# Optimization experiments

Hardware: AMD Instinct MI355X
Metric: run time of the kernel (lower is better)

The kernel has to match this reference:

```python
import jax, jax.numpy as jnp
import numpy as np

B, T, C = 2, 2048, 1024
H, D = 16, 64


def setup_inputs() -> dict:
    key = jax.random.key(0)
    k1, k2, k3 = jax.random.split(key, 3)
    x = jax.random.normal(k1, (B, T, C), dtype=jnp.float32)
    w_qkv = jax.random.normal(k2, (C, 3 * H * D), dtype=jnp.float32) * (C ** -0.5)
    w_proj = jax.random.normal(k3, (H * D, C), dtype=jnp.float32) * ((H * D) ** -0.5)
    sink_logit = jnp.zeros((H,), dtype=jnp.float32)
    return {"x": x, "w_qkv": w_qkv, "w_proj": w_proj, "sink_logit": sink_logit}


def reference(x, w_qkv, w_proj, sink_logit):
    b, t, c = x.shape
    qkv = x @ w_qkv                                  # [B,T,3HD]
    q, k, v = jnp.split(qkv, 3, axis=-1)
    # [B,H,T,D]
    q = q.reshape(b, t, H, D).transpose(0, 2, 1, 3)
    k = k.reshape(b, t, H, D).transpose(0, 2, 1, 3)
    v = v.reshape(b, t, H, D).transpose(0, 2, 1, 3)

    scale = 1.0 / jnp.sqrt(jnp.asarray(D, dtype=x.dtype))
    scores = jnp.einsum('bhqd,bhkd->bhqk', q, k) * scale   # [B,H,T,T]
    neg_inf = jnp.finfo(x.dtype).min
    causal = jnp.tril(jnp.ones((t, t), dtype=bool))
    scores = jnp.where(causal[None, None], scores, neg_inf)

    # sink column: per-head learnable logit b (added post-scale, V is zero)
    sink = jnp.broadcast_to(sink_logit.reshape(1, H, 1, 1), (b, H, t, 1)).astype(x.dtype)
    aug = jnp.concatenate([sink, scores], axis=-1)          # [B,H,T,T+1]
    attn = jax.nn.softmax(aug, axis=-1)
    # sink V is zero, so drop the sink column for the value contraction
    y = jnp.einsum('bhqk,bhkd->bhqd', attn[..., 1:], v)     # [B,H,T,D]
    y = y.transpose(0, 2, 1, 3).reshape(b, t, H * D)
    return y @ w_proj
```

## Files before the change

### kernel.cpp

```cpp
#include <hip/hip_runtime.h>
#include <hip/hip_bf16.h>
#include <stdint.h>

#define B_ 2
#define T_ 2048
#define C_ 1024
#define H_ 16
#define D_ 64

typedef __attribute__((ext_vector_type(8))) short short8;
typedef __attribute__((ext_vector_type(4))) float floatx4;

__device__ __forceinline__ float bf2f(uint16_t b) {
    return __uint_as_float(((uint32_t)b) << 16);
}
__device__ __forceinline__ uint16_t f2b(float f) {
    __hip_bfloat16 h = __float2bfloat16(f);
    return *(uint16_t*)&h;
}
__device__ __forceinline__ float exp2v(float x) {
    float r;
    asm("v_exp_f32 %0, %1" : "=v"(r) : "v"(x));
    return r;
}
__device__ __forceinline__ uint32_t cvtpk(float lo, float hi) {
    uint32_t r;
    asm("v_cvt_pk_bf16_f32 %0, %1, %2" : "=v"(r) : "v"(lo), "v"(hi));
    return r;
}
__device__ __forceinline__ void glds16(const uint16_t* g, uint16_t* l) {
    __builtin_amdgcn_global_load_lds(
        (const __attribute__((address_space(1))) uint32_t*)g,
        (__attribute__((address_space(3))) uint32_t*)l, 16, 0, 0);
}

__global__ void prep(const float* __restrict__ x, uint16_t* __restrict__ x_c,
                     const float* __restrict__ w_qkv, uint16_t* __restrict__ wt_qkv,
                     const float* __restrict__ w_proj, uint16_t* __restrict__ wt_proj) {
    __shared__ uint16_t tile[32][33];
    int id = blockIdx.x;
    int tid = threadIdx.x;
    if (id < 4096) {
        int i = (id * 256 + tid) * 4;
        float4 v = *(const float4*)(x + i);
        x_c[i + 0] = f2b(v.x);
        x_c[i + 1] = f2b(v.y);
        x_c[i + 2] = f2b(v.z);
        x_c[i + 3] = f2b(v.w);
        return;
    }
    const float* in;
    uint16_t* out;
    int R, W, bx, by;
    if (id < 7168) {
        int tb = id - 4096;
        in = w_qkv; out = wt_qkv; R = 1024; W = 3072;
        bx = tb % 96; by = tb / 96;
    } else {
        int tb = id - 7168;
        in = w_proj; out = wt_proj; R = 1024; W = 1024;
        bx = tb & 31; by = tb >> 5;
    }
    int tx = tid & 31, ty = tid >> 5;
    int c0 = bx * 32, r0 = by * 32;
    #pragma unroll
    for (int i = 0; i < 32; i += 8)
        tile[ty + i][tx] = f2b(in[(size_t)(r0 + ty + i) * W + (c0 + tx)]);
    __syncthreads();
    #pragma unroll
    for (int i = 0; i < 32; i += 8)
        out[(size_t)(c0 + ty + i) * R + (r0 + tx)] = tile[tx][ty + i];
}

template <bool OUT_F32>
__global__ __launch_bounds__(256, 3)
void gemm_bt(const uint16_t* __restrict__ A, const uint16_t* __restrict__ Bt,
             void* __restrict__ Cv, int M, int N, int K) {
    __shared__ uint16_t As[3][128][32];
    __shared__ uint16_t Bs[3][128][32];
    int tid = threadIdx.x;
    int w = tid >> 6, lane = tid & 63;
    int quad = lane >> 4, l16 = lane & 15;
    int wr = (w >> 1) * 64, wc = (w & 1) * 64;

    int nwg = gridDim.x;
    int wg = (blockIdx.x & 7) * (nwg >> 3) + (blockIdx.x >> 3);
    int nby = N >> 7;
    int row0 = (wg / nby) * 128;
    int col0 = (wg % nby) * 128;

    int sr = w * 32 + (lane >> 2);
    int gsc = ((lane & 3) ^ ((lane >> 2) & 3)) * 8;
    uint16_t* lA0 = &As[0][sr][(lane & 3) * 8];
    uint16_t* lB0 = &Bs[0][sr][(lane & 3) * 8];
    const uint16_t* gA = A + (size_t)(row0 + sr) * K + gsc;
    const uint16_t* gB = Bt + (size_t)(col0 + sr) * K + gsc;

    floatx4 acc[4][4];
    #pragma unroll
    for (int i = 0; i < 4; i++)
        #pragma unroll
        for (int j = 0; j < 4; j++)
            acc[i][j] = (floatx4){0.f, 0.f, 0.f, 0.f};

#define STAGE3_(bs_, t_)                                                    \
    {                                                                       \
        const uint16_t* ga_ = gA + (size_t)(t_) * 32;                       \
        const uint16_t* gb_ = gB + (size_t)(t_) * 32;                       \
        uint16_t* la_ = lA0 + (bs_) * 4096;                                 \
        uint16_t* lb_ = lB0 + (bs_) * 4096;                                 \
        glds16(ga_, la_);                                                   \
        glds16(ga_ + 16 * K, la_ + 512);                                    \
        glds16(gb_, lb_);                                                   \
        glds16(gb_ + 16 * K, lb_ + 512);                                    \
    }

    int NT = K >> 5;
    STAGE3_(0, 0);
    STAGE3_(1, 1);
    asm volatile("s_waitcnt vmcnt(4)" ::: "memory");
    __builtin_amdgcn_s_barrier();

    const uint16_t* Ab = &As[0][0][0];
    const uint16_t* Bb = &Bs[0][0][0];
    int s = (quad ^ (l16 & 3)) * 8;
    int bc = 0, bs = 2;
    for (int t = 0; t < NT; ++t) {
        if (t + 2 < NT) STAGE3_(bs, t + 2);
        __builtin_amdgcn_sched_barrier(0);
        const uint16_t* Ac = Ab + bc * 4096;
        const uint16_t* Bc = Bb + bc * 4096;
        short8 af[4], bfr[4];
        #pragma unroll
        for (int i = 0; i < 4; i++)
            af[i] = *(const short8*)&Ac[(wr + i * 16 + l16) * 32 + s];
        #pragma unroll
        for (int j = 0; j < 4; j++)
            bfr[j] = *(const short8*)&Bc[(wc + j * 16 + l16) * 32 + s];
        #pragma unroll
        for (int i = 0; i < 4; i++)
            #pragma unroll
            for (int j = 0; j < 4; j++)
                acc[i][j] = __builtin_amdgcn_mfma_f32_16x16x32_bf16(
                    af[i], bfr[j], acc[i][j], 0, 0, 0);
        if (t + 2 < NT) {
            asm volatile("s_waitcnt vmcnt(4)" ::: "memory");
        } else {
            asm volatile("s_waitcnt vmcnt(0)" ::: "memory");
        }
        __builtin_amdgcn_s_barrier();
        bc = (bc == 2) ? 0 : bc + 1;
        bs = (bs == 2) ? 0 : bs + 1;
    }
#undef STAGE3_

    #pragma unroll
    for (int i = 0; i < 4; i++) {
        #pragma unroll
        for (int j = 0; j < 4; j++) {
            int rbase = row0 + wr + i * 16 + quad * 4;
            int cg = col0 + wc + j * 16 + l16;
            #pragma unroll
            for (int r = 0; r < 4; r++) {
                if (OUT_F32)
                    ((float*)Cv)[(size_t)(rbase + r) * N + cg] = acc[i][j][r];
                else
                    ((uint16_t*)Cv)[(size_t)(rbase + r) * N + cg] = f2b(acc[i][j][r]);
            }
        }
    }
}

__global__ __launch_bounds__(256, 2)
void attn_mfma(const uint16_t* __restrict__ qkv,
               const float* __restrict__ sink,
               uint16_t* __restrict__ y) {
    __shared__ uint16_t Ks[2][64][72];
    __shared__ uint16_t Vt[2][64][72];
    __shared__ uint16_t Pl[4][32][72];

    int tid = threadIdx.x;
    int w = tid >> 6, lane = tid & 63;
    int quad = lane >> 4, l16 = lane & 15;

    int id = blockIdx.x;
    int pair = id >> 5, bh = id & 31;
    int b = bh >> 4, h = bh & 15;
    int hi = 31 - pair, lo = pair;
    int q0s[2];
    q0s[0] = hi * 64 + w * 16;
    q0s[1] = lo * 64 + w * 16;
    int ktiles = hi + 1;
    int myk1 = lo + 1;

    const uint16_t* qkv_b = qkv + (size_t)b * T_ * 3072;

    const float QSC = 0.125f * 1.44269504f;
    short8 qf[2][2];
    #pragma unroll
    for (int qt = 0; qt < 2; qt++) {
        int qrow = q0s[qt] + l16;
        #pragma unroll
        for (int kd = 0; kd < 2; kd++) {
            uint4 raw = *(const uint4*)(qkv_b + (size_t)qrow * 3072 + h * 64 +
                                        kd * 32 + quad * 8);
            const uint16_t* rp = (const uint16_t*)&raw;
            short8 f;
            #pragma unroll
            for (int j = 0; j < 8; j++)
                f[j] = (short)f2b(bf2f(rp[j]) * QSC);
            qf[qt][kd] = f;
        }
    }

    float m_s[2], l_s[2];
    m_s[0] = m_s[1] = sink[h] * 1.44269504f;
    l_s[0] = l_s[1] = 1.0f;
    floatx4 acc_o[2][4];
    #pragma unroll
    for (int qt = 0; qt < 2; qt++)
        #pragma unroll
        for (int dt = 0; dt < 4; dt++)
            acc_o[qt][dt] = (floatx4){0.f, 0.f, 0.f, 0.f};

    int t2 = tid >> 3;
    int dg = tid & 7;
    const uint16_t* kgp = qkv_b + 1024 + h * 64 + (size_t)(2 * t2) * 3072 + dg * 8;
    const uint16_t* vgp = kgp + 1024;
    int vcw = 2 * (t2 ^ (4 * dg));

    uint4 kr0 = *(const uint4*)(kgp);
    uint4 kr1 = *(const uint4*)(kgp + 3072);
    uint4 vr0 = *(const uint4*)(vgp);
    uint4 vr1 = *(const uint4*)(vgp + 3072);
    {
        *(uint4*)&Ks[0][2 * t2][dg * 8] = kr0;
        *(uint4*)&Ks[0][2 * t2 + 1][dg * 8] = kr1;
        const uint16_t* a0 = (const uint16_t*)&vr0;
        const uint16_t* a1 = (const uint16_t*)&vr1;
        #pragma unroll
        for (int j = 0; j < 8; j++)
            *(uint32_t*)&Vt[0][dg * 8 + j][vcw] =
                (uint32_t)a0[j] | ((uint32_t)a1[j] << 16);
    }
    if (ktiles > 1) {
        kr0 = *(const uint4*)(kgp + 64 * 3072);
        kr1 = *(const uint4*)(kgp + 64 * 3072 + 3072);
        vr0 = *(const uint4*)(vgp + 64 * 3072);
        vr1 = *(const uint4*)(vgp + 64 * 3072 + 3072);
    }
    __syncthreads();

    for (int kt = 0; kt < ktiles; kt++) {
        int cur = kt & 1;
        if (kt + 1 < ktiles) {
            *(uint4*)&Ks[cur ^ 1][2 * t2][dg * 8] = kr0;
            *(uint4*)&Ks[cur ^ 1][2 * t2 + 1][dg * 8] = kr1;
            const uint16_t* a0 = (const uint16_t*)&vr0;
            const uint16_t* a1 = (const uint16_t*)&vr1;
            #pragma unroll
            for (int j = 0; j < 8; j++)
                *(uint32_t*)&Vt[cur ^ 1][dg * 8 + j][vcw] =
                    (uint32_t)a0[j] | ((uint32_t)a1[j] << 16);
        }
        if (kt + 2 < ktiles) {
            size_t off = (size_t)(kt + 2) * 64 * 3072;
            kr0 = *(const uint4*)(kgp + off);
            kr1 = *(const uint4*)(kgp + off + 3072);
            vr0 = *(const uint4*)(vgp + off);
            vr1 = *(const uint4*)(vgp + off + 3072);
        }
        short8 kf[4][2];
        #pragma unroll
        for (int rt = 0; rt < 4; rt++) {
            kf[rt][0] = *(const short8*)&Ks[cur][rt * 16 + l16][quad * 8];
            kf[rt][1] = *(const short8*)&Ks[cur][rt * 16 + l16][32 + quad * 8];
        }
        short8 vf[2][4];
        #pragma unroll
        for (int kb = 0; kb < 2; kb++)
            #pragma unroll
            for (int dt = 0; dt < 4; dt++) {
                int d = dt * 16 + l16;
                int col = 2 * (((kb * 16) + quad * 4) ^ (4 * (d >> 3)));
                vf[kb][dt] = *(const short8*)&Vt[cur][d][col];
            }
        #pragma unroll
        for (int qt = 0; qt < 2; qt++) {
            if (qt == 1 && kt >= myk1) continue;
            floatx4 acc_s[4];
            #pragma unroll
            for (int rt = 0; rt < 4; rt++)
                acc_s[rt] = (floatx4){0.f, 0.f, 0.f, 0.f};
            #pragma unroll
            for (int rt = 0; rt < 4; rt++) {
                acc_s[rt] = __builtin_amdgcn_mfma_f32_16x16x32_bf16(
                    kf[rt][0], qf[qt][0], acc_s[rt], 0, 0, 0);
                acc_s[rt] = __builtin_amdgcn_mfma_f32_16x16x32_bf16(
                    kf[rt][1], qf[qt][1], acc_s[rt], 0, 0, 0);
            }
            int dqt = (qt == 0) ? hi : lo;
            if (kt == dqt) {
                int qg = q0s[qt] + l16;
                #pragma unroll
                for (int rt = 0; rt < 4; rt++) {
                    int kg = kt * 64 + rt * 16 + quad * 4;
                    #pragma unroll
                    for (int r = 0; r < 4; r++)
                        if (kg + r > qg) acc_s[rt][r] = -1e30f;
                }
            }
            float mx = -1e30f;
            #pragma unroll
            for (int rt = 0; rt < 4; rt++)
                #pragma unroll
                for (int r = 0; r < 4; r++) mx = fmaxf(mx, acc_s[rt][r]);
            mx = fmaxf(mx, __shfl_xor(mx, 16));
            mx = fmaxf(mx, __shfl_xor(mx, 32));
            float mold = m_s[qt];
            if (!__all(mx <= mold + 8.0f)) {
                float mnew = fmaxf(mold, mx);
                float alpha = exp2v(mold - mnew);
                m_s[qt] = mnew;
                l_s[qt] *= alpha;
                #pragma unroll
                for (int r = 0; r < 4; r++) {
                    float ar = __shfl(alpha, (lane & 48) | (quad * 4 + r));
                    #pragma unroll
                    for (int dt = 0; dt < 4; dt++) acc_o[qt][dt][r] *= ar;
                }
            }
            float mcur = m_s[qt];
            float psum = 0.f;
            #pragma unroll
            for (int rt = 0; rt < 4; rt++) {
                float p0 = exp2v(acc_s[rt][0] - mcur);
                float p1 = exp2v(acc_s[rt][1] - mcur);
                float p2 = exp2v(acc_s[rt][2] - mcur);
                float p3 = exp2v(acc_s[rt][3] - mcur);
                psum += (p0 + p1) + (p2 + p3);
                uint2 pk;
                pk.x = cvtpk(p0, p1);
                pk.y = cvtpk(p2, p3);
                *(uint2*)&Pl[w][qt * 16 + l16][rt * 16 + quad * 4] = pk;
            }
            psum += __shfl_xor(psum, 16);
            psum += __shfl_xor(psum, 32);
            l_s[qt] += psum;
            #pragma unroll
            for (int kb = 0; kb < 2; kb++) {
                short8 pf = *(const short8*)&Pl[w][qt * 16 + l16][kb * 32 + quad * 8];
                #pragma unroll
                for (int dt = 0; dt < 4; dt++)
                    acc_o[qt][dt] = __builtin_amdgcn_mfma_f32_16x16x32_bf16(
                        pf, vf[kb][dt], acc_o[qt][dt], 0, 0, 0);
            }
        }
        __syncthreads();
    }

    #pragma unroll
    for (int qt = 0; qt < 2; qt++) {
        #pragma unroll
        for (int r = 0; r < 4; r++) {
            float lr = __shfl(l_s[qt], (lane & 48) | (quad * 4 + r));
            float inv = 1.0f / lr;
            int qg = q0s[qt] + quad * 4 + r;
            uint16_t* yp = y + (size_t)(b * T_ + qg) * 1024 + h * 64;
            #pragma unroll
            for (int dt = 0; dt < 4; dt++)
                yp[dt * 16 + l16] = f2b(acc_o[qt][dt][r] * inv);
        }
    }
}

extern "C" void kernel_launch(void* const* d_in, const int* in_sizes, int n_in,
                              void* d_out, int out_size, void* d_ws, size_t ws_size,
                              hipStream_t stream) {
    const float* x      = (const float*)d_in[0];
    const float* w_qkv  = (const float*)d_in[1];
    const float* w_proj = (const float*)d_in[2];
    const float* sink   = (const float*)d_in[3];
    float* out          = (float*)d_out;

    char* ws = (char*)d_ws;
    uint16_t* wt_qkv  = (uint16_t*)ws;
    uint16_t* wt_proj = (uint16_t*)(ws + 6291456);
    uint16_t* x_c     = (uint16_t*)(ws + 8388608);
    uint16_t* qkv     = (uint16_t*)(ws + 16777216);
    uint16_t* yb      = (uint16_t*)(ws + 41943040);

    prep<<<dim3(8192), 256, 0, stream>>>(x, x_c, w_qkv, wt_qkv, w_proj, wt_proj);

    gemm_bt<false><<<dim3(768), 256, 0, stream>>>(
        x_c, wt_qkv, qkv, 4096, 3072, 1024);

    attn_mfma<<<dim3(16 * 32), 256, 0, stream>>>(qkv, sink, yb);

    gemm_bt<true><<<dim3(256), 256, 0, stream>>>(
        yb, wt_proj, out, 4096, 1024, 1024);
}
```

Before: 181.1 us.

## Split attention into per-strip blocks and narrow projection GEMM tiles

The attention kernel no longer pairs a high and a low query strip per block. It launches one block per 64-row strip, heaviest strips first, which doubles the grid, halves per-thread accumulator state and the P scratch buffer, and raises the occupancy hint to 3. The output projection GEMM gains a BN template parameter and runs with 128x64 tiles on 512 blocks instead of 256, so the small GEMM fills more CUs. The risk is that attention now relies on launch order rather than explicit pairing for load balance, and the narrower GEMM tile gets less B-operand reuse.

```diff
diff --git a/kernel.cpp b/kernel.cpp
--- a/kernel.cpp
+++ b/kernel.cpp
@@ -72,35 +72,39 @@
         out[(size_t)(c0 + ty + i) * R + (r0 + tx)] = tile[tx][ty + i];
 }
 
-template <bool OUT_F32>
+template <bool OUT_F32, int BN>
 __global__ __launch_bounds__(256, 3)
 void gemm_bt(const uint16_t* __restrict__ A, const uint16_t* __restrict__ Bt,
              void* __restrict__ Cv, int M, int N, int K) {
+    constexpr int NJ = BN / 32;
+    constexpr int BUFB = BN * 32;
     __shared__ uint16_t As[3][128][32];
-    __shared__ uint16_t Bs[3][128][32];
+    __shared__ uint16_t Bs[3][BN][32];
     int tid = threadIdx.x;
     int w = tid >> 6, lane = tid & 63;
     int quad = lane >> 4, l16 = lane & 15;
-    int wr = (w >> 1) * 64, wc = (w & 1) * 64;
+    int wr = (w >> 1) * 64, wc = (w & 1) * (BN / 2);
 
     int nwg = gridDim.x;
     int wg = (blockIdx.x & 7) * (nwg >> 3) + (blockIdx.x >> 3);
-    int nby = N >> 7;
+    int nby = N / BN;
     int row0 = (wg / nby) * 128;
-    int col0 = (wg % nby) * 128;
+    int col0 = (wg % nby) * BN;
 
     int sr = w * 32 + (lane >> 2);
-    int gsc = ((lane & 3) ^ ((lane >> 2) & 3)) * 8;
+    int gscA = ((lane & 3) ^ ((lane >> 2) & 3)) * 8;
     uint16_t* lA0 = &As[0][sr][(lane & 3) * 8];
-    uint16_t* lB0 = &Bs[0][sr][(lane & 3) * 8];
-    const uint16_t* gA = A + (size_t)(row0 + sr) * K + gsc;
-    const uint16_t* gB = Bt + (size_t)(col0 + sr) * K + gsc;
-
-    floatx4 acc[4][4];
+    const uint16_t* gA = A + (size_t)(row0 + sr) * K + gscA;
+    int srB = (BN == 128) ? sr : (tid >> 2);
+    int gscB = ((lane & 3) ^ (srB & 3)) * 8;
+    uint16_t* lB0 = &Bs[0][srB][(lane & 3) * 8];
+    const uint16_t* gB = Bt + (size_t)(col0 + srB) * K + gscB;
+
+    floatx4 acc[4][NJ];
     #pragma unroll
     for (int i = 0; i < 4; i++)
         #pragma unroll
-        for (int j = 0; j < 4; j++)
+        for (int j = 0; j < NJ; j++)
             acc[i][j] = (floatx4){0.f, 0.f, 0.f, 0.f};
 
 #define STAGE3_(bs_, t_)                                                    \
@@ -108,17 +112,20 @@
         const uint16_t* ga_ = gA + (size_t)(t_) * 32;                       \
         const uint16_t* gb_ = gB + (size_t)(t_) * 32;                       \
         uint16_t* la_ = lA0 + (bs_) * 4096;                                 \
-        uint16_t* lb_ = lB0 + (bs_) * 4096;                                 \
+        uint16_t* lb_ = lB0 + (bs_) * BUFB;                                 \
         glds16(ga_, la_);                                                   \
         glds16(ga_ + 16 * K, la_ + 512);                                    \
         glds16(gb_, lb_);                                                   \
-        glds16(gb_ + 16 * K, lb_ + 512);                                    \
+        if constexpr (BN == 128) glds16(gb_ + 16 * K, lb_ + 512);           \
     }
 
     int NT = K >> 5;
     STAGE3_(0, 0);
     STAGE3_(1, 1);
-    asm volatile("s_waitcnt vmcnt(4)" ::: "memory");
+    if constexpr (BN == 128)
+        asm volatile("s_waitcnt vmcnt(4)" ::: "memory");
+    else
+        asm volatile("s_waitcnt vmcnt(3)" ::: "memory");
     __builtin_amdgcn_s_barrier();
 
     const uint16_t* Ab = &As[0][0][0];
@@ -129,22 +136,25 @@
         if (t + 2 < NT) STAGE3_(bs, t + 2);
         __builtin_amdgcn_sched_barrier(0);
         const uint16_t* Ac = Ab + bc * 4096;
-        const uint16_t* Bc = Bb + bc * 4096;
-        short8 af[4], bfr[4];
+        const uint16_t* Bc = Bb + bc * BUFB;
+        short8 af[4], bfr[NJ];
         #pragma unroll
         for (int i = 0; i < 4; i++)
             af[i] = *(const short8*)&Ac[(wr + i * 16 + l16) * 32 + s];
         #pragma unroll
-        for (int j = 0; j < 4; j++)
+        for (int j = 0; j < NJ; j++)
             bfr[j] = *(const short8*)&Bc[(wc + j * 16 + l16) * 32 + s];
         #pragma unroll
         for (int i = 0; i < 4; i++)
             #pragma unroll
-            for (int j = 0; j < 4; j++)
+            for (int j = 0; j < NJ; j++)
                 acc[i][j] = __builtin_amdgcn_mfma_f32_16x16x32_bf16(
                     af[i], bfr[j], acc[i][j], 0, 0, 0);
         if (t + 2 < NT) {
-            asm volatile("s_waitcnt vmcnt(4)" ::: "memory");
+            if constexpr (BN == 128)
+                asm volatile("s_waitcnt vmcnt(4)" ::: "memory");
+            else
+                asm volatile("s_waitcnt vmcnt(3)" ::: "memory");
         } else {
             asm volatile("s_waitcnt vmcnt(0)" ::: "memory");
         }
@@ -157,7 +167,7 @@
     #pragma unroll
     for (int i = 0; i < 4; i++) {
         #pragma unroll
-        for (int j = 0; j < 4; j++) {
+        for (int j = 0; j < NJ; j++) {
             int rbase = row0 + wr + i * 16 + quad * 4;
             int cg = col0 + wc + j * 16 + l16;
             #pragma unroll
@@ -171,35 +181,31 @@
     }
 }
 
-__global__ __launch_bounds__(256, 2)
+__global__ __launch_bounds__(256, 3)
 void attn_mfma(const uint16_t* __restrict__ qkv,
                const float* __restrict__ sink,
                uint16_t* __restrict__ y) {
     __shared__ uint16_t Ks[2][64][72];
     __shared__ uint16_t Vt[2][64][72];
-    __shared__ uint16_t Pl[4][32][72];
+    __shared__ uint16_t Pl[4][16][72];
 
     int tid = threadIdx.x;
     int w = tid >> 6, lane = tid & 63;
     int quad = lane >> 4, l16 = lane & 15;
 
     int id = blockIdx.x;
-    int pair = id >> 5, bh = id & 31;
+    int strip = 31 - (id >> 5);
+    int bh = id & 31;
     int b = bh >> 4, h = bh & 15;
-    int hi = 31 - pair, lo = pair;
-    int q0s[2];
-    q0s[0] = hi * 64 + w * 16;
-    q0s[1] = lo * 64 + w * 16;
-    int ktiles = hi + 1;
-    int myk1 = lo + 1;
+    int q0 = strip * 64 + w * 16;
+    int ktiles = strip + 1;
 
     const uint16_t* qkv_b = qkv + (size_t)b * T_ * 3072;
 
     const float QSC = 0.125f * 1.44269504f;
-    short8 qf[2][2];
-    #pragma unroll
-    for (int qt = 0; qt < 2; qt++) {
-        int qrow = q0s[qt] + l16;
+    short8 qf[2];
+    {
+        int qrow = q0 + l16;
         #pragma unroll
         for (int kd = 0; kd < 2; kd++) {
             uint4 raw = *(const uint4*)(qkv_b + (size_t)qrow * 3072 + h * 64 +
@@ -209,19 +215,16 @@
             #pragma unroll
             for (int j = 0; j < 8; j++)
                 f[j] = (short)f2b(bf2f(rp[j]) * QSC);
-            qf[qt][kd] = f;
-        }
-    }
-
-    float m_s[2], l_s[2];
-    m_s[0] = m_s[1] = sink[h] * 1.44269504f;
-    l_s[0] = l_s[1] = 1.0f;
-    floatx4 acc_o[2][4];
-    #pragma unroll
-    for (int qt = 0; qt < 2; qt++)
-        #pragma unroll
-        for (int dt = 0; dt < 4; dt++)
-            acc_o[qt][dt] = (floatx4){0.f, 0.f, 0.f, 0.f};
+            qf[kd] = f;
+        }
+    }
+
+    float m_s = sink[h] * 1.44269504f;
+    float l_s = 1.0f;
+    floatx4 acc_o[4];
+    #pragma unroll
+    for (int dt = 0; dt < 4; dt++)
+        acc_o[dt] = (floatx4){0.f, 0.f, 0.f, 0.f};
 
     int t2 = tid >> 3;
     int dg = tid & 7;
@@ -285,92 +288,84 @@
                 int col = 2 * (((kb * 16) + quad * 4) ^ (4 * (d >> 3)));
                 vf[kb][dt] = *(const short8*)&Vt[cur][d][col];
             }
-        #pragma unroll
-        for (int qt = 0; qt < 2; qt++) {
-            if (qt == 1 && kt >= myk1) continue;
-            floatx4 acc_s[4];
-            #pragma unroll
-            for (int rt = 0; rt < 4; rt++)
-                acc_s[rt] = (floatx4){0.f, 0.f, 0.f, 0.f};
+        floatx4 acc_s[4];
+        #pragma unroll
+        for (int rt = 0; rt < 4; rt++)
+            acc_s[rt] = (floatx4){0.f, 0.f, 0.f, 0.f};
+        #pragma unroll
+        for (int rt = 0; rt < 4; rt++) {
+            acc_s[rt] = __builtin_amdgcn_mfma_f32_16x16x32_bf16(
+                kf[rt][0], qf[0], acc_s[rt], 0, 0, 0);
+            acc_s[rt] = __builtin_amdgcn_mfma_f32_16x16x32_bf16(
+                kf[rt][1], qf[1], acc_s[rt], 0, 0, 0);
+        }
+        if (kt == strip) {
+            int qg = q0 + l16;
             #pragma unroll
             for (int rt = 0; rt < 4; rt++) {
-                acc_s[rt] = __builtin_amdgcn_mfma_f32_16x16x32_bf16(
-                    kf[rt][0], qf[qt][0], acc_s[rt], 0, 0, 0);
-                acc_s[rt] = __builtin_amdgcn_mfma_f32_16x16x32_bf16(
-                    kf[rt][1], qf[qt][1], acc_s[rt], 0, 0, 0);
+                int kg = kt * 64 + rt * 16 + quad * 4;
+                #pragma unroll
+                for (int r = 0; r < 4; r++)
+                    if (kg + r > qg) acc_s[rt][r] = -1e30f;
             }
-            int dqt = (qt == 0) ? hi : lo;
-            if (kt == dqt) {
-                int qg = q0s[qt] + l16;
+        }
+        float mx = -1e30f;
+        #pragma unroll
+        for (int rt = 0; rt < 4; rt++)
+            #pragma unroll
+            for (int r = 0; r < 4; r++) mx = fmaxf(mx, acc_s[rt][r]);
+        mx = fmaxf(mx, __shfl_xor(mx, 16));
+        mx = fmaxf(mx, __shfl_xor(mx, 32));
+        float mold = m_s;
+        if (!__all(mx <= mold + 8.0f)) {
+            float mnew = fmaxf(mold, mx);
+            float alpha = exp2v(mold - mnew);
+            m_s = mnew;
+            l_s *= alpha;
+            #pragma unroll
+            for (int r = 0; r < 4; r++) {
+                float ar = __shfl(alpha, (lane & 48) | (quad * 4 + r));
                 #pragma unroll
-                for (int rt = 0; rt < 4; rt++) {
-                    int kg = kt * 64 + rt * 16 + quad * 4;
-                    #pragma unroll
-                    for (int r = 0; r < 4; r++)
-                        if (kg + r > qg) acc_s[rt][r] = -1e30f;
-                }
+                for (int dt = 0; dt < 4; dt++) acc_o[dt][r] *= ar;
             }
-            float mx = -1e30f;
-            #pragma unroll
-            for (int rt = 0; rt < 4; rt++)
-                #pragma unroll
-                for (int r = 0; r < 4; r++) mx = fmaxf(mx, acc_s[rt][r]);
-            mx = fmaxf(mx, __shfl_xor(mx, 16));
-            mx = fmaxf(mx, __shfl_xor(mx, 32));
-            float mold = m_s[qt];
-            if (!__all(mx <= mold + 8.0f)) {
-                float mnew = fmaxf(mold, mx);
-                float alpha = exp2v(mold - mnew);
-                m_s[qt] = mnew;
-                l_s[qt] *= alpha;
-                #pragma unroll
-                for (int r = 0; r < 4; r++) {
-                    float ar = __shfl(alpha, (lane & 48) | (quad * 4 + r));
-                    #pragma unroll
-                    for (int dt = 0; dt < 4; dt++) acc_o[qt][dt][r] *= ar;
-                }
-            }
-            float mcur = m_s[qt];
-            float psum = 0.f;
-            #pragma unroll
-            for (int rt = 0; rt < 4; rt++) {
-                float p0 = exp2v(acc_s[rt][0] - mcur);
-                float p1 = exp2v(acc_s[rt][1] - mcur);
-                float p2 = exp2v(acc_s[rt][2] - mcur);
-                float p3 = exp2v(acc_s[rt][3] - mcur);
-                psum += (p0 + p1) + (p2 + p3);
-                uint2 pk;
-                pk.x = cvtpk(p0, p1);
-                pk.y = cvtpk(p2, p3);
-                *(uint2*)&Pl[w][qt * 16 + l16][rt * 16 + quad * 4] = pk;
-            }
-            psum += __shfl_xor(psum, 16);
-            psum += __shfl_xor(psum, 32);
-            l_s[qt] += psum;
-            #pragma unroll
-            for (int kb = 0; kb < 2; kb++) {
-                short8 pf = *(const short8*)&Pl[w][qt * 16 + l16][kb * 32 + quad * 8];
-                #pragma unroll
-                for (int dt = 0; dt < 4; dt++)
-                    acc_o[qt][dt] = __builtin_amdgcn_mfma_f32_16x16x32_bf16(
-                        pf, vf[kb][dt], acc_o[qt][dt], 0, 0, 0);
-            }
+        }
+        float mcur = m_s;
+        float psum = 0.f;
+        #pragma unroll
+        for (int rt = 0; rt < 4; rt++) {
+            float p0 = exp2v(acc_s[rt][0] - mcur);
+            float p1 = exp2v(acc_s[rt][1] - mcur);
+            float p2 = exp2v(acc_s[rt][2] - mcur);
+            float p3 = exp2v(acc_s[rt][3] - mcur);
+            psum += (p0 + p1) + (p2 + p3);
+            uint2 pk;
+            pk.x = cvtpk(p0, p1);
+            pk.y = cvtpk(p2, p3);
+            *(uint2*)&Pl[w][l16][rt * 16 + quad * 4] = pk;
+        }
+        psum += __shfl_xor(psum, 16);
+        psum += __shfl_xor(psum, 32);
+        l_s += psum;
+        #pragma unroll
+        for (int kb = 0; kb < 2; kb++) {
+            short8 pf = *(const short8*)&Pl[w][l16][kb * 32 + quad * 8];
+            #pragma unroll
+            for (int dt = 0; dt < 4; dt++)
+                acc_o[dt] = __builtin_amdgcn_mfma_f32_16x16x32_bf16(
+                    pf, vf[kb][dt], acc_o[dt], 0, 0, 0);
         }
         __syncthreads();
     }
 
     #pragma unroll
-    for (int qt = 0; qt < 2; qt++) {
-        #pragma unroll
-        for (int r = 0; r < 4; r++) {
-            float lr = __shfl(l_s[qt], (lane & 48) | (quad * 4 + r));
-            float inv = 1.0f / lr;
-            int qg = q0s[qt] + quad * 4 + r;
-            uint16_t* yp = y + (size_t)(b * T_ + qg) * 1024 + h * 64;
-            #pragma unroll
-            for (int dt = 0; dt < 4; dt++)
-                yp[dt * 16 + l16] = f2b(acc_o[qt][dt][r] * inv);
-        }
+    for (int r = 0; r < 4; r++) {
+        float lr = __shfl(l_s, (lane & 48) | (quad * 4 + r));
+        float inv = 1.0f / lr;
+        int qg = q0 + quad * 4 + r;
+        uint16_t* yp = y + (size_t)(b * T_ + qg) * 1024 + h * 64;
+        #pragma unroll
+        for (int dt = 0; dt < 4; dt++)
+            yp[dt * 16 + l16] = f2b(acc_o[dt][r] * inv);
     }
 }
 
@@ -392,11 +387,11 @@
 
     prep<<<dim3(8192), 256, 0, stream>>>(x, x_c, w_qkv, wt_qkv, w_proj, wt_proj);
 
-    gemm_bt<false><<<dim3(768), 256, 0, stream>>>(
+    gemm_bt<false, 128><<<dim3(768), 256, 0, stream>>>(
         x_c, wt_qkv, qkv, 4096, 3072, 1024);
 
-    attn_mfma<<<dim3(16 * 32), 256, 0, stream>>>(qkv, sink, yb);
-
-    gemm_bt<true><<<dim3(256), 256, 0, stream>>>(
+    attn_mfma<<<dim3(32 * 32), 256, 0, stream>>>(qkv, sink, yb);
+
+    gemm_bt<true, 64><<<dim3(512), 256, 0, stream>>>(
         yb, wt_proj, out, 4096, 1024, 1024);
 }
```

Result: faster. 177.0 us (-2.3%).
